# Kernel optimization log

Measured on AMD Instinct MI355X. Metric: run time of the kernel, lower is better.

The kernel has to match this reference:

```python
import jax, jax.numpy as jnp
import numpy as np

D_MODEL = 1024
N_HEADS = 16
B, T = 16, 512


def setup_inputs() -> dict:
    key = jax.random.key(0)
    ks = jax.random.split(key, 5)
    s = 0.02
    return {
        "x": jax.random.normal(ks[0], (B, T, D_MODEL), dtype=jnp.float32),
        "w_qkv": jax.random.normal(ks[1], (D_MODEL, 3 * D_MODEL), dtype=jnp.float32) * s,
        "b_qkv": jax.random.normal(ks[2], (3 * D_MODEL,), dtype=jnp.float32) * s,
        "w_o": jax.random.normal(ks[3], (D_MODEL, D_MODEL), dtype=jnp.float32) * s,
        "b_o": jax.random.normal(ks[4], (D_MODEL,), dtype=jnp.float32) * s,
    }


def reference(x, w_qkv, b_qkv, w_o, b_o):
    Bx, Tx, C = x.shape
    H = N_HEADS
    hd = C // H
    qkv = x @ w_qkv + b_qkv                      # [B,T,3C]
    qkv = qkv.reshape(Bx, Tx, 3, H, hd).transpose(2, 0, 3, 1, 4)  # [3,B,H,T,hd]
    q, k, v = qkv[0], qkv[1], qkv[2]
    # NOTE: original scales by sqrt(C) = sqrt(d_model), not sqrt(head_dim)
    att = jnp.einsum("bhqd,bhkd->bhqk", q, k) / jnp.sqrt(jnp.float32(C))
    causal = jnp.tril(jnp.ones((Tx, Tx), dtype=bool))
    att = jnp.where(causal, att, -jnp.inf)
    att = jax.nn.softmax(att, axis=-1)
    y = jnp.einsum("bhqk,bhkd->bhqd", att, v)    # [B,H,T,hd]
    y = y.transpose(0, 2, 1, 3).reshape(Bx, Tx, C)
    return y @ w_o + b_o
```

## Files before the change

kernel.cpp:

```cpp
#include <hip/hip_runtime.h>
#include <cstddef>


#define B_  16
#define T_  512
#define C_  1024
#define H_  16
#define HD_ 64

typedef __bf16 bf16x8 __attribute__((ext_vector_type(8)));
typedef float  f32x4  __attribute__((ext_vector_type(4)));

__device__ __forceinline__ void gload16(const void* g, void* lds_dst) {
  __builtin_amdgcn_global_load_lds(
      (const __attribute__((address_space(1))) unsigned int*)g,
      (__attribute__((address_space(3))) unsigned int*)lds_dst, 16, 0, 0);
}

__global__ void cvt_kernel(const float* __restrict__ in, __bf16* __restrict__ out, int n) {
  int i = (blockIdx.x * 256 + threadIdx.x) * 8;
  if (i >= n) return;
  float4 f0 = *(const float4*)&in[i];
  float4 f1 = *(const float4*)&in[i + 4];
  bf16x8 o;
  o[0] = (__bf16)f0.x; o[1] = (__bf16)f0.y; o[2] = (__bf16)f0.z; o[3] = (__bf16)f0.w;
  o[4] = (__bf16)f1.x; o[5] = (__bf16)f1.y; o[6] = (__bf16)f1.z; o[7] = (__bf16)f1.w;
  *(bf16x8*)&out[i] = o;
}

__global__ void tconv_kernel(const float* __restrict__ w, __bf16* __restrict__ wt,
                             int K, int N) {
  __shared__ float tile[32][33];
  int tx = threadIdx.x, ty = threadIdx.y;
  int n0 = blockIdx.x * 32, k0 = blockIdx.y * 32;
  #pragma unroll
  for (int i = 0; i < 4; ++i) {
    int r = ty + i * 8;
    tile[r][tx] = w[(size_t)(k0 + r) * N + n0 + tx];
  }
  __syncthreads();
  #pragma unroll
  for (int i = 0; i < 4; ++i) {
    int r = ty + i * 8;
    wt[(size_t)(n0 + r) * K + k0 + tx] = (__bf16)tile[tx][r];
  }
}

__global__ __launch_bounds__(256) void gemmsq_kernel(
    const __bf16* __restrict__ A, const __bf16* __restrict__ BT,
    const float* __restrict__ bias, int K, int NBn,
    __bf16* __restrict__ oq, __bf16* __restrict__ okk, __bf16* __restrict__ ovt)
{
  __shared__ __attribute__((aligned(16))) char lds[32768];
  const int tid = threadIdx.x, lane = tid & 63, wid = tid >> 6;
  const int wm = wid >> 1, wn = wid & 1;
  const int lr = lane & 15, lg = lane >> 4;

  const int cpx = gridDim.x >> 3;
  const int id = (blockIdx.x & 7) * cpx + (blockIdx.x >> 3);
  const int m0 = (id / NBn) * 128, n0 = (id % NBn) * 128;

  const int r8  = wid * 8 + (lane >> 3);
  const int csw = ((lane & 7) ^ (lane >> 3)) * 8;

  auto stage = [&](const __bf16* g, char* dst) {
    #pragma unroll
    for (int i = 0; i < 4; ++i)
      gload16(g + (size_t)(i * 32 + r8) * K + csw, dst + i * 4096 + wid * 1024);
  };
  auto rd = [&](bf16x8* d, const char* buf, int woff) {
    #pragma unroll
    for (int f = 0; f < 4; ++f) {
      const char* rp = buf + (woff + f * 16 + lr) * 128;
      #pragma unroll
      for (int ks = 0; ks < 2; ++ks)
        d[f * 2 + ks] = *(const bf16x8*)(rp + (((ks << 2) + lg) ^ (lr & 7)) * 16);
    }
  };

  f32x4 acc[4][4] = {};
  const int nt = K >> 6;
  const __bf16* gA = A  + (size_t)m0 * K;
  const __bf16* gB = BT + (size_t)n0 * K;
  char* const Ab = lds;
  char* const Bb = lds + 16384;

  stage(gA, Ab);
  stage(gB, Bb);
  asm volatile("s_waitcnt vmcnt(0)\ns_barrier" ::: "memory");

  bf16x8 a[8], b[8];
  for (int t = 0; t < nt; ++t) {
    rd(a, Ab, wm * 64);
    rd(b, Bb, wn * 64);
    asm volatile("s_waitcnt lgkmcnt(0)\ns_barrier" ::: "memory");
    if (t + 1 < nt) {
      stage(gA + (size_t)(t + 1) * 64, Ab);
      stage(gB + (size_t)(t + 1) * 64, Bb);
    }
    __builtin_amdgcn_s_setprio(1);
    #pragma unroll
    for (int mf = 0; mf < 4; ++mf)
      #pragma unroll
      for (int nf = 0; nf < 4; ++nf)
        #pragma unroll
        for (int ks = 0; ks < 2; ++ks)
          acc[mf][nf] = __builtin_amdgcn_mfma_f32_16x16x32_bf16(
              a[mf * 2 + ks], b[nf * 2 + ks], acc[mf][nf], 0, 0, 0);
    __builtin_amdgcn_s_setprio(0);
    asm volatile("s_waitcnt vmcnt(0)\ns_barrier" ::: "memory");
  }

  const float QSC = 0.04508422f;
  #pragma unroll
  for (int nf = 0; nf < 4; ++nf) {
    int n = n0 + wn * 64 + nf * 16 + lr;
    float bv = bias[n];
    int which = n >> 10;
    int h = (n >> 6) & 15, d = n & 63;
    if (which == 2) {
      #pragma unroll
      for (int mf = 0; mf < 4; ++mf) {
        int m = m0 + wm * 64 + mf * 16 + lg * 4;
        int bb = m >> 9, t0 = m & 511;
        ushort4 pk;
        __bf16 e0 = (__bf16)(acc[mf][nf][0] + bv);
        __bf16 e1 = (__bf16)(acc[mf][nf][1] + bv);
        __bf16 e2 = (__bf16)(acc[mf][nf][2] + bv);
        __bf16 e3 = (__bf16)(acc[mf][nf][3] + bv);
        pk.x = *(unsigned short*)&e0; pk.y = *(unsigned short*)&e1;
        pk.z = *(unsigned short*)&e2; pk.w = *(unsigned short*)&e3;
        *(ushort4*)&ovt[(size_t)((bb * H_ + h) * HD_ + d) * T_ + t0] = pk;
      }
    } else {
      __bf16* dst = (which == 0) ? oq : okk;
      const float scl = (which == 0) ? QSC : 1.0f;
      #pragma unroll
      for (int mf = 0; mf < 4; ++mf)
        #pragma unroll
        for (int j = 0; j < 4; ++j) {
          int m = m0 + wm * 64 + mf * 16 + lg * 4 + j;
          int bb = m >> 9, tt = m & 511;
          dst[(size_t)((bb * H_ + h) * T_ + tt) * HD_ + d] =
              (__bf16)((acc[mf][nf][j] + bv) * scl);
        }
    }
  }
}

__global__ __launch_bounds__(256) void gemmsq_o_kernel(
    const __bf16* __restrict__ A, const __bf16* __restrict__ BT,
    const float* __restrict__ bias, int K, int NBn, int N,
    float* __restrict__ out32)
{
  __shared__ __attribute__((aligned(16))) char lds[24576];
  const int tid = threadIdx.x, lane = tid & 63, wid = tid >> 6;
  const int wm = wid >> 1, wn = wid & 1;
  const int lr = lane & 15, lg = lane >> 4;

  const int cpx = gridDim.x >> 3;
  const int id = (blockIdx.x & 7) * cpx + (blockIdx.x >> 3);
  const int m0 = (id / NBn) * 64, n0 = (id % NBn) * 128;

  const int r8  = wid * 8 + (lane >> 3);
  const int csw = ((lane & 7) ^ (lane >> 3)) * 8;

  auto stageA = [&](const __bf16* g, char* dst) {
    #pragma unroll
    for (int i = 0; i < 2; ++i)
      gload16(g + (size_t)(i * 32 + r8) * K + csw, dst + i * 4096 + wid * 1024);
  };
  auto stageB = [&](const __bf16* g, char* dst) {
    #pragma unroll
    for (int i = 0; i < 4; ++i)
      gload16(g + (size_t)(i * 32 + r8) * K + csw, dst + i * 4096 + wid * 1024);
  };
  auto rdA = [&](bf16x8* d, const char* buf) {
    #pragma unroll
    for (int f = 0; f < 2; ++f) {
      const char* rp = buf + (wm * 32 + f * 16 + lr) * 128;
      #pragma unroll
      for (int ks = 0; ks < 2; ++ks)
        d[f * 2 + ks] = *(const bf16x8*)(rp + (((ks << 2) + lg) ^ (lr & 7)) * 16);
    }
  };
  auto rdB = [&](bf16x8* d, const char* buf) {
    #pragma unroll
    for (int f = 0; f < 4; ++f) {
      const char* rp = buf + (wn * 64 + f * 16 + lr) * 128;
      #pragma unroll
      for (int ks = 0; ks < 2; ++ks)
        d[f * 2 + ks] = *(const bf16x8*)(rp + (((ks << 2) + lg) ^ (lr & 7)) * 16);
    }
  };

  f32x4 acc[2][4] = {};
  const int nt = K >> 6;
  const __bf16* gA = A  + (size_t)m0 * K;
  const __bf16* gB = BT + (size_t)n0 * K;
  char* const Ab = lds;
  char* const Bb = lds + 8192;

  stageA(gA, Ab);
  stageB(gB, Bb);
  asm volatile("s_waitcnt vmcnt(0)\ns_barrier" ::: "memory");

  bf16x8 a[4], b[8];
  for (int t = 0; t < nt; ++t) {
    rdA(a, Ab);
    rdB(b, Bb);
    asm volatile("s_waitcnt lgkmcnt(0)\ns_barrier" ::: "memory");
    if (t + 1 < nt) {
      stageA(gA + (size_t)(t + 1) * 64, Ab);
      stageB(gB + (size_t)(t + 1) * 64, Bb);
    }
    __builtin_amdgcn_s_setprio(1);
    #pragma unroll
    for (int mf = 0; mf < 2; ++mf)
      #pragma unroll
      for (int nf = 0; nf < 4; ++nf)
        #pragma unroll
        for (int ks = 0; ks < 2; ++ks)
          acc[mf][nf] = __builtin_amdgcn_mfma_f32_16x16x32_bf16(
              a[mf * 2 + ks], b[nf * 2 + ks], acc[mf][nf], 0, 0, 0);
    __builtin_amdgcn_s_setprio(0);
    asm volatile("s_waitcnt vmcnt(0)\ns_barrier" ::: "memory");
  }

  #pragma unroll
  for (int nf = 0; nf < 4; ++nf) {
    int n = n0 + wn * 64 + nf * 16 + lr;
    float bv = bias[n];
    #pragma unroll
    for (int mf = 0; mf < 2; ++mf)
      #pragma unroll
      for (int j = 0; j < 4; ++j) {
        int m = m0 + wm * 32 + mf * 16 + lg * 4 + j;
        out32[(size_t)m * N + n] = acc[mf][nf][j] + bv;
      }
  }
}

__global__ __launch_bounds__(512) void attn_kernel(
    const __bf16* __restrict__ qb, const __bf16* __restrict__ kb,
    const __bf16* __restrict__ vtb, __bf16* __restrict__ y)
{
  extern __shared__ __align__(16) char smem[];
  char* const Ksb = smem;
  char* const Vtb = smem + 65536;
  char* const Psb = smem + 131072;

  const int tid = threadIdx.x, lane = tid & 63, w = tid >> 6;
  const int lr = lane & 15, lg = lane >> 4;
  const int bh = blockIdx.x;
  const size_t base = (size_t)bh * T_ * HD_;
  const int b = bh >> 4, h = bh & 15;

  {
    const int rk = tid >> 3;
    const int sk = (tid & 7) ^ (rk & 7);
    const int rv = tid >> 6;
    const int sv = (tid & 63) ^ rv;
    #pragma unroll
    for (int i = 0; i < 8; ++i) {
      gload16(kb  + base + (size_t)(i * 64 + rk) * HD_ + sk * 8,
              Ksb + i * 8192 + w * 1024);
      gload16(vtb + base + (size_t)(i * 8 + rv) * T_ + sv * 8,
              Vtb + i * 8192 + w * 1024);
    }
  }
  asm volatile("s_waitcnt vmcnt(0)\ns_barrier" ::: "memory");

  bf16x8 onesf;
  #pragma unroll
  for (int i = 0; i < 8; ++i) onesf[i] = (__bf16)1.0f;

  char* const PsW0 = Psb + (w * 2 + 0) * 2048;
  char* const PsW1 = Psb + (w * 2 + 1) * 2048;

  #pragma unroll 1
  for (int sw = 0; sw < 2; ++sw) {
    const int GA = sw * 16 + w;
    const int GB = sw * 16 + 15 - w;
    const int q0A = GA * 16, q0B = GB * 16;
    const int cA = GA >> 2, cB = GB >> 2;

    bf16x8 qfA[2], qfB[2];
    #pragma unroll
    for (int s = 0; s < 2; ++s) {
      qfA[s] = *(const bf16x8*)&qb[base + (size_t)(q0A + lr) * HD_ + s * 32 + lg * 8];
      qfB[s] = *(const bf16x8*)&qb[base + (size_t)(q0B + lr) * HD_ + s * 32 + lg * 8];
    }

    f32x4 accA[4] = {}, accB[4] = {};
    f32x4 saccA = {}, saccB = {};

    for (int c = 0; c <= cB; ++c) {
      const bool actA = (c <= cA);

      bf16x8 kf[2][4];
      #pragma unroll
      for (int s = 0; s < 2; ++s)
        #pragma unroll
        for (int cc = 0; cc < 4; ++cc)
          kf[s][cc] = *(const bf16x8*)(Ksb + (size_t)(c * 64 + cc * 16 + lr) * 128
                                       + (((s << 2) + lg) ^ (lr & 7)) * 16);

      #pragma unroll
      for (int g = 0; g < 2; ++g) {
        if (g == 0 && !actA) continue;
        const bf16x8* qf = (g == 0) ? qfA : qfB;
        const int q0 = (g == 0) ? q0A : q0B;
        const int cg = (g == 0) ? cA : cB;
        char* PsW = (g == 0) ? PsW0 : PsW1;

        f32x4 sc[4] = {};
        __builtin_amdgcn_s_setprio(1);
        #pragma unroll
        for (int s = 0; s < 2; ++s)
          #pragma unroll
          for (int cc = 0; cc < 4; ++cc)
            sc[cc] = __builtin_amdgcn_mfma_f32_16x16x32_bf16(
                kf[s][cc], qf[s], sc[cc], 0, 0, 0);
        __builtin_amdgcn_s_setprio(0);

        #pragma unroll
        for (int cc = 0; cc < 4; ++cc) {
          float p[4];
          #pragma unroll
          for (int j = 0; j < 4; ++j) {
            float v = exp2f(sc[cc][j]);
            if (c == cg) {
              int kv = c * 64 + cc * 16 + lg * 4 + j;
              if (kv > q0 + lr) v = 0.f;
            }
            p[j] = v;
          }
          ushort4 pkw;
          __bf16 e0 = (__bf16)p[0], e1 = (__bf16)p[1];
          __bf16 e2 = (__bf16)p[2], e3 = (__bf16)p[3];
          pkw.x = *(unsigned short*)&e0; pkw.y = *(unsigned short*)&e1;
          pkw.z = *(unsigned short*)&e2; pkw.w = *(unsigned short*)&e3;
          int g16 = (2 * cc + (lg >> 1)) ^ (lr & 7);
          *(ushort4*)(PsW + lr * 128 + g16 * 16 + (lg & 1) * 8) = pkw;
        }
      }

      bf16x8 vf[2][4];
      #pragma unroll
      for (int s = 0; s < 2; ++s)
        #pragma unroll
        for (int dd = 0; dd < 4; ++dd)
          vf[s][dd] = *(const bf16x8*)(Vtb + (size_t)(dd * 16 + lr) * 1024
                                       + (8 * c + (((s << 2) + lg) ^ (lr & 7))) * 16);

      __builtin_amdgcn_s_setprio(1);
      #pragma unroll
      for (int g = 0; g < 2; ++g) {
        if (g == 0 && !actA) continue;
        char* PsW = (g == 0) ? PsW0 : PsW1;
        f32x4* acc = (g == 0) ? accA : accB;
        f32x4& sacc = (g == 0) ? saccA : saccB;
        #pragma unroll
        for (int s = 0; s < 2; ++s) {
          bf16x8 pa = *(const bf16x8*)(PsW + lr * 128
                                       + (((s << 2) + lg) ^ (lr & 7)) * 16);
          sacc = __builtin_amdgcn_mfma_f32_16x16x32_bf16(pa, onesf, sacc, 0, 0, 0);
          #pragma unroll
          for (int dd = 0; dd < 4; ++dd)
            acc[dd] = __builtin_amdgcn_mfma_f32_16x16x32_bf16(
                pa, vf[s][dd], acc[dd], 0, 0, 0);
        }
      }
      __builtin_amdgcn_s_setprio(0);
    }

    #pragma unroll
    for (int g = 0; g < 2; ++g) {
      const int q0 = (g == 0) ? q0A : q0B;
      f32x4* acc = (g == 0) ? accA : accB;
      f32x4& sacc = (g == 0) ? saccA : saccB;
      float inv[4];
      #pragma unroll
      for (int j = 0; j < 4; ++j) inv[j] = 1.f / sacc[j];
      #pragma unroll
      for (int dd = 0; dd < 4; ++dd)
        #pragma unroll
        for (int j = 0; j < 4; ++j) {
          int t = q0 + lg * 4 + j;
          int d = dd * 16 + lr;
          y[((size_t)(b * T_ + t)) * C_ + h * HD_ + d] = (__bf16)(acc[dd][j] * inv[j]);
        }
    }
  }
}

extern "C" void kernel_launch(void* const* d_in, const int* in_sizes, int n_in,
                              void* d_out, int out_size, void* d_ws, size_t ws_size,
                              hipStream_t stream) {
  const float* x    = (const float*)d_in[0];
  const float* wqkv = (const float*)d_in[1];
  const float* bqkv = (const float*)d_in[2];
  const float* wo   = (const float*)d_in[3];
  const float* bo   = (const float*)d_in[4];
  float* out = (float*)d_out;

  char* ws = (char*)d_ws;
  const size_t MB = 1u << 20;
  __bf16* xb    = (__bf16*)(ws);
  __bf16* wqt   = (__bf16*)(ws + 16 * MB);
  __bf16* wot   = (__bf16*)(ws + 22 * MB);
  __bf16* qbuf  = (__bf16*)(ws + 24 * MB);
  __bf16* kbuf  = (__bf16*)(ws + 40 * MB);
  __bf16* vtbuf = (__bf16*)(ws + 56 * MB);
  __bf16* ybuf  = (__bf16*)(ws + 72 * MB);

  (void)hipFuncSetAttribute(reinterpret_cast<const void*>(&attn_kernel),
                            hipFuncAttributeMaxDynamicSharedMemorySize, 163840);

  const int NX = B_ * T_ * C_;
  cvt_kernel<<<NX / (256 * 8), 256, 0, stream>>>(x, xb, NX);
  tconv_kernel<<<dim3(3 * C_ / 32, C_ / 32), dim3(32, 8), 0, stream>>>(wqkv, wqt, C_, 3 * C_);
  tconv_kernel<<<dim3(C_ / 32, C_ / 32), dim3(32, 8), 0, stream>>>(wo, wot, C_, C_);

  gemmsq_kernel<<<1536, 256, 0, stream>>>(
      xb, wqt, bqkv, C_, 24, qbuf, kbuf, vtbuf);

  attn_kernel<<<256, 512, 163840, stream>>>(qbuf, kbuf, vtbuf, ybuf);

  gemmsq_o_kernel<<<1024, 256, 0, stream>>>(
      ybuf, wot, bo, C_, 8, C_, out);
}
```

Before: 125.4 us.

## Rewrite QKV GEMM as 256x256 8-wave tile with multi-stage LDS pipeline

Replaces the 128x128, 4-wave QKV projection GEMM with a 256x256 tile computed by 8 waves. It uses double-buffered A and triple-buffered B in 160KB of dynamic LDS, and global loads are interleaved between four MFMA phases with two-deep prefetch. The goal is more data reuse per tile and better overlap of memory loads with MFMA work. In exchange the grid shrinks to 384 blocks, occupancy is capped by the large LDS footprint, and the hand-tuned waitcnt and barrier schedule is fragile.

After: 146.4 us. 1.17x slower.

```diff
diff --git a/kernel.cpp b/kernel.cpp
--- a/kernel.cpp
+++ b/kernel.cpp
@@ -46,70 +46,118 @@
   }
 }
 
-__global__ __launch_bounds__(256) void gemmsq_kernel(
+__global__ __launch_bounds__(512, 2) void gemmq8_kernel(
     const __bf16* __restrict__ A, const __bf16* __restrict__ BT,
     const float* __restrict__ bias, int K, int NBn,
     __bf16* __restrict__ oq, __bf16* __restrict__ okk, __bf16* __restrict__ ovt)
 {
-  __shared__ __attribute__((aligned(16))) char lds[32768];
+  extern __shared__ __align__(16) char lds[];
   const int tid = threadIdx.x, lane = tid & 63, wid = tid >> 6;
-  const int wm = wid >> 1, wn = wid & 1;
+  const int wm = wid >> 2, wn = wid & 3;
   const int lr = lane & 15, lg = lane >> 4;
 
   const int cpx = gridDim.x >> 3;
   const int id = (blockIdx.x & 7) * cpx + (blockIdx.x >> 3);
-  const int m0 = (id / NBn) * 128, n0 = (id % NBn) * 128;
-
-  const int r8  = wid * 8 + (lane >> 3);
-  const int csw = ((lane & 7) ^ (lane >> 3)) * 8;
-
-  auto stage = [&](const __bf16* g, char* dst) {
-    #pragma unroll
-    for (int i = 0; i < 4; ++i)
-      gload16(g + (size_t)(i * 32 + r8) * K + csw, dst + i * 4096 + wid * 1024);
-  };
-  auto rd = [&](bf16x8* d, const char* buf, int woff) {
+  const int m0 = (id / NBn) * 256, n0 = (id % NBn) * 256;
+
+  const int r8  = tid >> 3;
+  const int csw = ((tid & 7) ^ ((tid >> 3) & 7)) * 8;
+
+  auto stage_slabs = [&](const __bf16* g, char* dst, int s0, int s1) {
+    gload16(g + (size_t)(s0 * 64 + r8) * K + csw, dst + s0 * 8192 + wid * 1024);
+    gload16(g + (size_t)(s1 * 64 + r8) * K + csw, dst + s1 * 8192 + wid * 1024);
+  };
+
+  auto rdA = [&](bf16x8* d, const char* Ab, int mh) {
     #pragma unroll
     for (int f = 0; f < 4; ++f) {
-      const char* rp = buf + (woff + f * 16 + lr) * 128;
+      const char* rp = Ab + (wm * 128 + (mh * 4 + f) * 16 + lr) * 128;
       #pragma unroll
       for (int ks = 0; ks < 2; ++ks)
         d[f * 2 + ks] = *(const bf16x8*)(rp + (((ks << 2) + lg) ^ (lr & 7)) * 16);
     }
   };
-
-  f32x4 acc[4][4] = {};
+  auto rdB = [&](bf16x8* d, const char* Bb, int nh) {
+    #pragma unroll
+    for (int f = 0; f < 2; ++f) {
+      const char* rp = Bb + (wn * 64 + (nh * 2 + f) * 16 + lr) * 128;
+      #pragma unroll
+      for (int ks = 0; ks < 2; ++ks)
+        d[f * 2 + ks] = *(const bf16x8*)(rp + (((ks << 2) + lg) ^ (lr & 7)) * 16);
+    }
+  };
+
+  f32x4 acc[8][4] = {};
+
+  auto mmq = [&](int mh, int nh, const bf16x8* av, const bf16x8* bv) {
+    __builtin_amdgcn_s_setprio(1);
+    #pragma unroll
+    for (int f = 0; f < 4; ++f)
+      #pragma unroll
+      for (int g2 = 0; g2 < 2; ++g2)
+        #pragma unroll
+        for (int ks = 0; ks < 2; ++ks)
+          acc[mh * 4 + f][nh * 2 + g2] = __builtin_amdgcn_mfma_f32_16x16x32_bf16(
+              av[f * 2 + ks], bv[g2 * 2 + ks], acc[mh * 4 + f][nh * 2 + g2], 0, 0, 0);
+    __builtin_amdgcn_s_setprio(0);
+  };
+
+#define PH_MID() do {                                                        \
+    asm volatile("s_barrier\ns_waitcnt lgkmcnt(0)" ::: "memory");            \
+    __builtin_amdgcn_sched_barrier(0); } while (0)
+#define PH_END() asm volatile("s_barrier" ::: "memory")
+
   const int nt = K >> 6;
   const __bf16* gA = A  + (size_t)m0 * K;
   const __bf16* gB = BT + (size_t)n0 * K;
-  char* const Ab = lds;
-  char* const Bb = lds + 16384;
-
-  stage(gA, Ab);
-  stage(gB, Bb);
-  asm volatile("s_waitcnt vmcnt(0)\ns_barrier" ::: "memory");
-
-  bf16x8 a[8], b[8];
+  char* const A0b = lds;
+  char* const A1b = lds + 32768;
+  char* const Bb0 = lds + 65536;
+
+  stage_slabs(gB, Bb0, 0, 1);           stage_slabs(gB, Bb0, 2, 3);
+  stage_slabs(gA, A0b, 0, 1);           stage_slabs(gA, A0b, 2, 3);
+  stage_slabs(gB + 64, Bb0 + 32768, 0, 1); stage_slabs(gB + 64, Bb0 + 32768, 2, 3);
+  stage_slabs(gA + 64, A1b, 0, 1);      stage_slabs(gA + 64, A1b, 2, 3);
+  asm volatile("s_waitcnt vmcnt(8)\ns_barrier" ::: "memory");
+
+  bf16x8 a0[8], a1[8], b0[4], b1[4];
+
   for (int t = 0; t < nt; ++t) {
-    rd(a, Ab, wm * 64);
-    rd(b, Bb, wn * 64);
-    asm volatile("s_waitcnt lgkmcnt(0)\ns_barrier" ::: "memory");
-    if (t + 1 < nt) {
-      stage(gA + (size_t)(t + 1) * 64, Ab);
-      stage(gB + (size_t)(t + 1) * 64, Bb);
-    }
-    __builtin_amdgcn_s_setprio(1);
-    #pragma unroll
-    for (int mf = 0; mf < 4; ++mf)
-      #pragma unroll
-      for (int nf = 0; nf < 4; ++nf)
-        #pragma unroll
-        for (int ks = 0; ks < 2; ++ks)
-          acc[mf][nf] = __builtin_amdgcn_mfma_f32_16x16x32_bf16(
-              a[mf * 2 + ks], b[nf * 2 + ks], acc[mf][nf], 0, 0, 0);
-    __builtin_amdgcn_s_setprio(0);
-    asm volatile("s_waitcnt vmcnt(0)\ns_barrier" ::: "memory");
-  }
+    char* const Ab = (t & 1) ? A1b : A0b;
+    char* const Bb = Bb0 + (t % 3) * 32768;
+    char* const Bw = Bb0 + ((t + 2) % 3) * 32768;
+    const __bf16* gA2 = gA + (size_t)(t + 2) * 64;
+    const __bf16* gB2 = gB + (size_t)(t + 2) * 64;
+    const bool st = (t + 2 < nt);
+
+    rdA(a0, Ab, 0);
+    rdB(b0, Bb, 0);
+    if (st) stage_slabs(gB2, Bw, 0, 1);
+    asm volatile("s_waitcnt lgkmcnt(8)" ::: "memory");
+    PH_MID();
+    mmq(0, 0, a0, b0);
+    PH_END();
+
+    rdB(b1, Bb, 1);
+    if (st) stage_slabs(gB2, Bw, 2, 3);
+    PH_MID();
+    mmq(0, 1, a0, b1);
+    PH_END();
+
+    rdA(a1, Ab, 1);
+    if (st) stage_slabs(gA2, Ab, 0, 2);
+    PH_MID();
+    mmq(1, 0, a1, b0);
+    PH_END();
+
+    if (st) stage_slabs(gA2, Ab, 1, 3);
+    PH_MID();
+    mmq(1, 1, a1, b1);
+    if (st) { asm volatile("s_waitcnt vmcnt(8)\ns_barrier" ::: "memory"); }
+    else    { asm volatile("s_waitcnt vmcnt(0)\ns_barrier" ::: "memory"); }
+  }
+#undef PH_MID
+#undef PH_END
 
   const float QSC = 0.04508422f;
   #pragma unroll
@@ -120,8 +168,8 @@
     int h = (n >> 6) & 15, d = n & 63;
     if (which == 2) {
       #pragma unroll
-      for (int mf = 0; mf < 4; ++mf) {
-        int m = m0 + wm * 64 + mf * 16 + lg * 4;
+      for (int mf = 0; mf < 8; ++mf) {
+        int m = m0 + wm * 128 + mf * 16 + lg * 4;
         int bb = m >> 9, t0 = m & 511;
         ushort4 pk;
         __bf16 e0 = (__bf16)(acc[mf][nf][0] + bv);
@@ -136,10 +184,10 @@
       __bf16* dst = (which == 0) ? oq : okk;
       const float scl = (which == 0) ? QSC : 1.0f;
       #pragma unroll
-      for (int mf = 0; mf < 4; ++mf)
+      for (int mf = 0; mf < 8; ++mf)
         #pragma unroll
         for (int j = 0; j < 4; ++j) {
-          int m = m0 + wm * 64 + mf * 16 + lg * 4 + j;
+          int m = m0 + wm * 128 + mf * 16 + lg * 4 + j;
           int bb = m >> 9, tt = m & 511;
           dst[(size_t)((bb * H_ + h) * T_ + tt) * HD_ + d] =
               (__bf16)((acc[mf][nf][j] + bv) * scl);
@@ -417,14 +465,16 @@
 
   (void)hipFuncSetAttribute(reinterpret_cast<const void*>(&attn_kernel),
                             hipFuncAttributeMaxDynamicSharedMemorySize, 163840);
+  (void)hipFuncSetAttribute(reinterpret_cast<const void*>(&gemmq8_kernel),
+                            hipFuncAttributeMaxDynamicSharedMemorySize, 163840);
 
   const int NX = B_ * T_ * C_;
   cvt_kernel<<<NX / (256 * 8), 256, 0, stream>>>(x, xb, NX);
   tconv_kernel<<<dim3(3 * C_ / 32, C_ / 32), dim3(32, 8), 0, stream>>>(wqkv, wqt, C_, 3 * C_);
   tconv_kernel<<<dim3(C_ / 32, C_ / 32), dim3(32, 8), 0, stream>>>(wo, wot, C_, C_);
 
-  gemmsq_kernel<<<1536, 256, 0, stream>>>(
-      xb, wqt, bqkv, C_, 24, qbuf, kbuf, vtbuf);
+  gemmq8_kernel<<<384, 512, 163840, stream>>>(
+      xb, wqt, bqkv, C_, 12, qbuf, kbuf, vtbuf);
 
   attn_kernel<<<256, 512, 163840, stream>>>(qbuf, kbuf, vtbuf, ybuf);
 
```
